# Kernel optimization log

Measured on AMD Instinct MI355X. Metric: run time of the kernel, lower is better.

Reference implementation:

```python
import jax, jax.numpy as jnp
import numpy as np

A, B, K = 8192, 8192, 10

def setup_inputs() -> dict:
    key = jax.random.key(0)
    k1, k2, k3 = jax.random.split(key, 3)
    W = jax.random.uniform(k1, (A, B), dtype=jnp.float32)      # similarity weights (a,b)
    P_l = jax.random.uniform(k2, (A, K), dtype=jnp.float32)    # left cluster probs (a,k)
    P_r = jax.random.uniform(k3, (B, K), dtype=jnp.float32)    # right cluster probs (b,k)
    clusters_p = jnp.ones((K,), dtype=jnp.float32) / K         # nn.Parameter ones(k)/k
    return {"W": W, "P_l": P_l, "P_r": P_r, "clusters_p": clusters_p}

def reference(W, P_l, P_r, clusters_p):
    # Original math: sum_{a,b,k} W[a,b] * (P_l[a,k] + P_r[b,k] - 2*P_l[a,k]*P_r[b,k]) / clusters_p[k]
    # Decomposes exactly (no (a,b,k) intermediate):
    row_sum = W.sum(axis=1)                 # (a,)
    col_sum = W.sum(axis=0)                 # (b,)
    term_l = row_sum @ P_l                  # (k,)  sum_a rowsum[a] * P_l[a,k]
    term_r = col_sum @ P_r                  # (k,)  sum_b colsum[b] * P_r[b,k]
    WPr = W @ P_r                           # (a,k)
    cross = jnp.sum(P_l * WPr, axis=0)      # (k,)  diag(P_l^T W P_r)
    per_cluster = term_l + term_r - 2.0 * cross
    return jnp.sum(per_cluster / clusters_p)
```

## Files before the change

kernel.cpp:

```cpp
#include <hip/hip_runtime.h>


constexpr int K     = 10;
constexpr int TM    = 32;
constexpr int BLOCK = 1024;
constexpr int P     = 4;

typedef float f4 __attribute__((ext_vector_type(4)));

__global__ void prcut_zero_out(float* out) {
    if (threadIdx.x == 0) out[0] = 0.0f;
}

__global__ __launch_bounds__(BLOCK) void prcut_main(
    const float* __restrict__ W,
    const float* __restrict__ Pl,
    const float* __restrict__ Pr,
    const float* __restrict__ cp,
    float* __restrict__ out,
    int Bn)
{
    float inv[K];
#pragma unroll
    for (int k = 0; k < K; ++k) inv[k] = 1.0f / cp[k];

    const int half = Bn >> 1;
    const int c0   = blockIdx.x * half + threadIdx.x * 4;
    const int a0   = blockIdx.y * TM;

    float pr[4][K];
    float rs[4];
#pragma unroll
    for (int j = 0; j < 4; ++j) {
        const float* p = Pr + (size_t)(c0 + j) * K;
        float s = 0.0f;
#pragma unroll
        for (int k = 0; k < K; ++k) {
            float v = p[k] * inv[k];
            pr[j][k] = v;
            s += v;
        }
        rs[j] = s;
    }

    const float* wp  = W + (size_t)a0 * Bn + c0;
    const float* wld = wp + (size_t)P * Bn;

    f4 wbuf[P];
#pragma unroll
    for (int i = 0; i < P; ++i)
        wbuf[i] = *reinterpret_cast<const f4*>(wp + (size_t)i * Bn);

    float acc = 0.0f;

#pragma unroll 4
    for (int r = 0; r < TM - P; ++r) {
        const float* plp = Pl + (size_t)(a0 + r) * K;
        float la = 0.0f;
#pragma unroll
        for (int k = 0; k < K; ++k) la = fmaf(plp[k], inv[k], la);

        float d0 = 0.f, d1 = 0.f, d2 = 0.f, d3 = 0.f;
#pragma unroll
        for (int k = 0; k < K; ++k) {
            const float plk = plp[k];
            d0 = fmaf(plk, pr[0][k], d0);
            d1 = fmaf(plk, pr[1][k], d1);
            d2 = fmaf(plk, pr[2][k], d2);
            d3 = fmaf(plk, pr[3][k], d3);
        }

        const int slot = r & (P - 1);
        const f4 w = wbuf[slot];
        wbuf[slot] = *reinterpret_cast<const f4*>(wld);
        wld += Bn;

        acc = fmaf(w.x, fmaf(-2.0f, d0, la + rs[0]), acc);
        acc = fmaf(w.y, fmaf(-2.0f, d1, la + rs[1]), acc);
        acc = fmaf(w.z, fmaf(-2.0f, d2, la + rs[2]), acc);
        acc = fmaf(w.w, fmaf(-2.0f, d3, la + rs[3]), acc);
    }

#pragma unroll
    for (int r = TM - P; r < TM; ++r) {
        const float* plp = Pl + (size_t)(a0 + r) * K;
        float la = 0.0f;
#pragma unroll
        for (int k = 0; k < K; ++k) la = fmaf(plp[k], inv[k], la);

        float d0 = 0.f, d1 = 0.f, d2 = 0.f, d3 = 0.f;
#pragma unroll
        for (int k = 0; k < K; ++k) {
            const float plk = plp[k];
            d0 = fmaf(plk, pr[0][k], d0);
            d1 = fmaf(plk, pr[1][k], d1);
            d2 = fmaf(plk, pr[2][k], d2);
            d3 = fmaf(plk, pr[3][k], d3);
        }

        const f4 w = wbuf[r & (P - 1)];
        acc = fmaf(w.x, fmaf(-2.0f, d0, la + rs[0]), acc);
        acc = fmaf(w.y, fmaf(-2.0f, d1, la + rs[1]), acc);
        acc = fmaf(w.z, fmaf(-2.0f, d2, la + rs[2]), acc);
        acc = fmaf(w.w, fmaf(-2.0f, d3, la + rs[3]), acc);
    }

#pragma unroll
    for (int off = 32; off > 0; off >>= 1)
        acc += __shfl_down(acc, off, 64);

    __shared__ float wsum[BLOCK / 64];
    const int lane = threadIdx.x & 63;
    const int wid  = threadIdx.x >> 6;
    if (lane == 0) wsum[wid] = acc;
    __syncthreads();

    if (threadIdx.x == 0) {
        float s = 0.0f;
#pragma unroll
        for (int i = 0; i < BLOCK / 64; ++i) s += wsum[i];
        atomicAdd(out, s);
    }
}

extern "C" void kernel_launch(void* const* d_in, const int* in_sizes, int n_in,
                              void* d_out, int out_size, void* d_ws, size_t ws_size,
                              hipStream_t stream) {
    const float* W  = (const float*)d_in[0];
    const float* Pl = (const float*)d_in[1];
    const float* Pr = (const float*)d_in[2];
    const float* cp = (const float*)d_in[3];
    float* out = (float*)d_out;

    const int Kn = in_sizes[3];
    const int A  = in_sizes[1] / Kn;
    const int B  = in_sizes[2] / Kn;

    prcut_zero_out<<<1, 64, 0, stream>>>(out);

    dim3 grid(2, A / TM);
    prcut_main<<<grid, BLOCK, 0, stream>>>(W, Pl, Pr, cp, out, B);
}
```

Baseline: 362.4 us.

## Precompute per-row Pl records in a prep kernel and narrow per-thread column width

Adds a prep kernel that computes, for each row, the weighted left sum and -2*Pl into a padded 12-float record in the workspace. This removes the per-row la reduction and the -2 scaling from the main loop. Each thread now handles 2 columns instead of 4, so the grid has more column blocks, and a minimum occupancy hint of 8 is added. W is read with nontemporal loads to avoid polluting the cache. In exchange there is an extra launch, extra workspace traffic, narrower vector loads, and Pr records are reread by more blocks.

```diff
diff --git a/kernel.cpp b/kernel.cpp
--- a/kernel.cpp
+++ b/kernel.cpp
@@ -2,41 +2,56 @@
 
 
 constexpr int K     = 10;
+constexpr int REC   = 12;
 constexpr int TM    = 32;
 constexpr int BLOCK = 1024;
+constexpr int COLS  = BLOCK * 2;
 constexpr int P     = 4;
 
-typedef float f4 __attribute__((ext_vector_type(4)));
+typedef float f2 __attribute__((ext_vector_type(2)));
 
-__global__ void prcut_zero_out(float* out) {
-    if (threadIdx.x == 0) out[0] = 0.0f;
+__global__ void prcut_prep(const float* __restrict__ Pl,
+                           const float* __restrict__ cp,
+                           float* __restrict__ rec,
+                           float* __restrict__ out, int A)
+{
+    const int a = blockIdx.x * blockDim.x + threadIdx.x;
+    if (a == 0) out[0] = 0.0f;
+    if (a >= A) return;
+    float la = 0.0f;
+    float r[REC];
+#pragma unroll
+    for (int k = 0; k < K; ++k) {
+        const float p = Pl[(size_t)a * K + k];
+        la = fmaf(p, 1.0f / cp[k], la);
+        r[1 + k] = -2.0f * p;
+    }
+    r[0] = la;
+    r[11] = 0.0f;
+#pragma unroll
+    for (int k = 0; k < REC; ++k) rec[(size_t)a * REC + k] = r[k];
 }
 
-__global__ __launch_bounds__(BLOCK) void prcut_main(
+__global__ __launch_bounds__(BLOCK, 8) void prcut_main(
     const float* __restrict__ W,
-    const float* __restrict__ Pl,
     const float* __restrict__ Pr,
     const float* __restrict__ cp,
+    const float* __restrict__ rec,
     float* __restrict__ out,
     int Bn)
 {
-    float inv[K];
+    const int c0 = blockIdx.x * COLS + threadIdx.x * 2;
+    const int a0 = blockIdx.y * TM;
+
+    float pr[2][K];
+    float rs[2];
 #pragma unroll
-    for (int k = 0; k < K; ++k) inv[k] = 1.0f / cp[k];
-
-    const int half = Bn >> 1;
-    const int c0   = blockIdx.x * half + threadIdx.x * 4;
-    const int a0   = blockIdx.y * TM;
-
-    float pr[4][K];
-    float rs[4];
-#pragma unroll
-    for (int j = 0; j < 4; ++j) {
+    for (int j = 0; j < 2; ++j) {
         const float* p = Pr + (size_t)(c0 + j) * K;
         float s = 0.0f;
 #pragma unroll
         for (int k = 0; k < K; ++k) {
-            float v = p[k] * inv[k];
+            const float v = p[k] * (1.0f / cp[k]);
             pr[j][k] = v;
             s += v;
         }
@@ -46,63 +61,52 @@
     const float* wp  = W + (size_t)a0 * Bn + c0;
     const float* wld = wp + (size_t)P * Bn;
 
-    f4 wbuf[P];
+    f2 wbuf[P];
 #pragma unroll
     for (int i = 0; i < P; ++i)
-        wbuf[i] = *reinterpret_cast<const f4*>(wp + (size_t)i * Bn);
+        wbuf[i] = __builtin_nontemporal_load(
+            reinterpret_cast<const f2*>(wp + (size_t)i * Bn));
 
     float acc = 0.0f;
+    const float* rp = rec + (size_t)a0 * REC;
 
 #pragma unroll 4
     for (int r = 0; r < TM - P; ++r) {
-        const float* plp = Pl + (size_t)(a0 + r) * K;
-        float la = 0.0f;
-#pragma unroll
-        for (int k = 0; k < K; ++k) la = fmaf(plp[k], inv[k], la);
-
-        float d0 = 0.f, d1 = 0.f, d2 = 0.f, d3 = 0.f;
+        const float la = rp[0];
+        float d0 = la + rs[0];
+        float d1 = la + rs[1];
 #pragma unroll
         for (int k = 0; k < K; ++k) {
-            const float plk = plp[k];
-            d0 = fmaf(plk, pr[0][k], d0);
-            d1 = fmaf(plk, pr[1][k], d1);
-            d2 = fmaf(plk, pr[2][k], d2);
-            d3 = fmaf(plk, pr[3][k], d3);
+            const float q = rp[1 + k];
+            d0 = fmaf(q, pr[0][k], d0);
+            d1 = fmaf(q, pr[1][k], d1);
         }
+        rp += REC;
 
         const int slot = r & (P - 1);
-        const f4 w = wbuf[slot];
-        wbuf[slot] = *reinterpret_cast<const f4*>(wld);
+        const f2 w = wbuf[slot];
+        wbuf[slot] = __builtin_nontemporal_load(
+            reinterpret_cast<const f2*>(wld));
         wld += Bn;
 
-        acc = fmaf(w.x, fmaf(-2.0f, d0, la + rs[0]), acc);
-        acc = fmaf(w.y, fmaf(-2.0f, d1, la + rs[1]), acc);
-        acc = fmaf(w.z, fmaf(-2.0f, d2, la + rs[2]), acc);
-        acc = fmaf(w.w, fmaf(-2.0f, d3, la + rs[3]), acc);
+        acc = fmaf(w.x, d0, fmaf(w.y, d1, acc));
     }
 
 #pragma unroll
     for (int r = TM - P; r < TM; ++r) {
-        const float* plp = Pl + (size_t)(a0 + r) * K;
-        float la = 0.0f;
-#pragma unroll
-        for (int k = 0; k < K; ++k) la = fmaf(plp[k], inv[k], la);
-
-        float d0 = 0.f, d1 = 0.f, d2 = 0.f, d3 = 0.f;
+        const float la = rp[0];
+        float d0 = la + rs[0];
+        float d1 = la + rs[1];
 #pragma unroll
         for (int k = 0; k < K; ++k) {
-            const float plk = plp[k];
-            d0 = fmaf(plk, pr[0][k], d0);
-            d1 = fmaf(plk, pr[1][k], d1);
-            d2 = fmaf(plk, pr[2][k], d2);
-            d3 = fmaf(plk, pr[3][k], d3);
+            const float q = rp[1 + k];
+            d0 = fmaf(q, pr[0][k], d0);
+            d1 = fmaf(q, pr[1][k], d1);
         }
+        rp += REC;
 
-        const f4 w = wbuf[r & (P - 1)];
-        acc = fmaf(w.x, fmaf(-2.0f, d0, la + rs[0]), acc);
-        acc = fmaf(w.y, fmaf(-2.0f, d1, la + rs[1]), acc);
-        acc = fmaf(w.z, fmaf(-2.0f, d2, la + rs[2]), acc);
-        acc = fmaf(w.w, fmaf(-2.0f, d3, la + rs[3]), acc);
+        const f2 w = wbuf[r & (P - 1)];
+        acc = fmaf(w.x, d0, fmaf(w.y, d1, acc));
     }
 
 #pragma unroll
@@ -131,13 +135,14 @@
     const float* Pr = (const float*)d_in[2];
     const float* cp = (const float*)d_in[3];
     float* out = (float*)d_out;
+    float* rec = (float*)d_ws;
 
     const int Kn = in_sizes[3];
     const int A  = in_sizes[1] / Kn;
     const int B  = in_sizes[2] / Kn;
 
-    prcut_zero_out<<<1, 64, 0, stream>>>(out);
+    prcut_prep<<<(A + 255) / 256, 256, 0, stream>>>(Pl, cp, rec, out, A);
 
-    dim3 grid(2, A / TM);
-    prcut_main<<<grid, BLOCK, 0, stream>>>(W, Pl, Pr, cp, out, B);
+    dim3 grid(B / COLS, A / TM);
+    prcut_main<<<grid, BLOCK, 0, stream>>>(W, Pr, cp, rec, out, B);
 }
```

Result: faster. 349.9 us (-3.4%).
